# Optimization experiments

Measured on AMD Instinct MI355X. Metric: run time of the kernel, lower is better.

The kernel has to match this reference:

```python
import jax, jax.numpy as jnp
import numpy as np

N_H = 256
N_LAYERS = 3
D_IN = 2  # concat([t, x], axis=1)


def setup_inputs() -> dict:
    key = jax.random.key(0)
    ks = jax.random.split(key, 20)
    N = 131072
    H, L = N_H, N_LAYERS

    def xavier(k, shape):
        fan_in, fan_out = shape[-2], shape[-1]
        limit = np.sqrt(6.0 / (fan_in + fan_out)).astype(np.float32)
        return jax.random.uniform(k, shape, jnp.float32, -limit, limit)

    inp = {
        "t": jax.random.uniform(ks[0], (N, 1), jnp.float32),
        "x": jax.random.normal(ks[1], (N, 1), jnp.float32),
        # initial dense layer: [2, H]
        "W0": xavier(ks[2], (D_IN, H)),
        "b0": jnp.zeros((1, H), jnp.float32),
        # stacked per-layer LSTM-like weights: U* [L, 2, H], W* [L, H, H], b* [L, 1, H]
        "Uz": xavier(ks[3], (L, D_IN, H)),
        "Ug": xavier(ks[4], (L, D_IN, H)),
        "Ur": xavier(ks[5], (L, D_IN, H)),
        "Uh": xavier(ks[6], (L, D_IN, H)),
        "Wz": xavier(ks[7], (L, H, H)),
        "Wg": xavier(ks[8], (L, H, H)),
        "Wr": xavier(ks[9], (L, H, H)),
        "Wh": xavier(ks[10], (L, H, H)),
        "bz": jnp.zeros((L, 1, H), jnp.float32),
        "bg": jnp.zeros((L, 1, H), jnp.float32),
        "br": jnp.zeros((L, 1, H), jnp.float32),
        "bh": jnp.zeros((L, 1, H), jnp.float32),
        # final dense layer: [H, 1]
        "Wf": xavier(ks[11], (H, 1)),
        "bf": jnp.zeros((1, 1), jnp.float32),
    }
    return inp


def _dgm_forward(t, x, W0, b0, Uz, Ug, Ur, Uh, Wz, Wg, Wr, Wh, bz, bg, br, bh, Wf, bf):
    X = jnp.concatenate([t, x], axis=1)            # [N, 2]
    S1 = jnp.tanh(X @ W0 + b0)                     # [N, H] -- initial state, held fixed

    def layer_step(S, params):
        uz, ug, ur, uh, wz, wg, wr, wh, pz, pg, pr, ph = params
        Z = jnp.tanh(X @ uz + S @ wz + pz)
        G = jnp.tanh(X @ ug + S1 @ wg + pg)
        R = jnp.tanh(X @ ur + S @ wr + pr)
        Hg = jnp.tanh(X @ uh + (S * R) @ wh + ph)
        Snew = (1.0 - G) * Hg + Z * S
        return Snew, None

    S, _ = jax.lax.scan(layer_step, S1, (Uz, Ug, Ur, Uh, Wz, Wg, Wr, Wh, bz, bg, br, bh))
    return S @ Wf + bf                             # [N, 1]


def reference(t, x, W0, b0, Uz, Ug, Ur, Uh, Wz, Wg, Wr, Wh, bz, bg, br, bh, Wf, bf):
    return _dgm_forward(t, x, W0, b0, Uz, Ug, Ur, Uh, Wz, Wg, Wr, Wh, bz, bg, br, bh, Wf, bf)
```

## Files before the change

### kernel.cpp

```cpp
#include <hip/hip_runtime.h>


typedef __attribute__((ext_vector_type(8))) short bf16x8;
typedef __attribute__((ext_vector_type(4))) float f32x4;

#if __has_builtin(__builtin_amdgcn_exp2f)
#define EXP2F(x) __builtin_amdgcn_exp2f(x)
#else
#define EXP2F(x) __expf((x) * 0.6931471805599453f)
#endif

__device__ __forceinline__ short f2bf(float f) {
    unsigned u = __float_as_uint(f);
    unsigned r = (u + 0x7FFFu + ((u >> 16) & 1u)) >> 16;
    return (short)r;
}
__device__ __forceinline__ float bf2f(short h) {
    return __uint_as_float(((unsigned)(unsigned short)h) << 16);
}
__device__ __forceinline__ unsigned cvtpk(float lo, float hi) {
    unsigned r;
    asm("v_cvt_pk_bf16_f32 %0, %1, %2" : "=v"(r) : "v"(lo), "v"(hi));
    return r;
}
__device__ __forceinline__ float rcp_1pe2x(float x) {
    float e = EXP2F(x * 2.8853900817779268f);
    return __builtin_amdgcn_rcpf(e + 1.0f);
}
__device__ __forceinline__ float fast_tanh(float x) {
    return fmaf(-2.0f, rcp_1pe2x(x), 1.0f);
}
__device__ __forceinline__ int sw_off(int r, int k) {
    return r * 256 + ((((k >> 3) ^ r) & 31) << 3) + (k & 7);
}
__device__ __forceinline__ unsigned pk2(float a, float b) { return cvtpk(a, b); }
__device__ __forceinline__ float upk(unsigned p, int hi) {
    return __uint_as_float(hi ? (p & 0xFFFF0000u) : (p << 16));
}

__global__ void pack_w(const float* __restrict__ Wz, const float* __restrict__ Wg,
                       const float* __restrict__ Wr, const float* __restrict__ Wh,
                       short* __restrict__ out) {
    __shared__ __align__(16) short lds[256 * 40];
    int mat = blockIdx.x >> 3;
    int kb  = blockIdx.x & 7;
    int l = mat >> 2, g = mat & 3;
    const float* W = (g == 0) ? Wz : (g == 1) ? Wg : (g == 2) ? Wr : Wh;
    const float* Wsl = W + l * 65536 + kb * 32 * 256;
    const int t = threadIdx.x;

#pragma unroll
    for (int j = 0; j < 8; j++) {
        int f  = j * 256 + t;
        int kp = f >> 6;
        int n0 = (f & 63) * 4;
        float4 v = ((const float4*)Wsl)[f];
        lds[(n0 + 0) * 40 + kp] = f2bf(v.x);
        lds[(n0 + 1) * 40 + kp] = f2bf(v.y);
        lds[(n0 + 2) * 40 + kp] = f2bf(v.z);
        lds[(n0 + 3) * 40 + kp] = f2bf(v.w);
    }
    __syncthreads();

    short* outm = out + mat * 65536;
#pragma unroll
    for (int j = 0; j < 4; j++) {
        int vp = j * 256 + t;
        int c  = vp >> 6;
        int ln = vp & 63;
        int n   = c * 16 + (ln & 15);
        int kp0 = (ln >> 4) * 8;
        bf16x8 val = *(const bf16x8*)(lds + n * 40 + kp0);
        *(bf16x8*)(outm + (((c * 8 + kb) * 64 + ln) << 3)) = val;
    }
}

__device__ __forceinline__ void gate_gemm(const short* __restrict__ In,
                                          const short* __restrict__ Wm,
                                          const float* __restrict__ U,
                                          const float* __restrict__ bias,
                                          const float2* __restrict__ txS,
                                          int q, int c15, int w,
                                          f32x4 acc[2][2]) {
    float2 tx[8];
#pragma unroll
    for (int rb = 0; rb < 2; rb++)
#pragma unroll
        for (int ii = 0; ii < 4; ii++) tx[rb * 4 + ii] = txS[rb * 16 + q * 4 + ii];
#pragma unroll
    for (int cb = 0; cb < 2; cb++) {
        int col = (w * 2 + cb) * 16 + c15;
        float u0 = U[col], u1 = U[256 + col], bb = bias[col];
#pragma unroll
        for (int rb = 0; rb < 2; rb++)
#pragma unroll
            for (int ii = 0; ii < 4; ii++)
                acc[rb][cb][ii] = bb + tx[rb * 4 + ii].x * u0 + tx[rb * 4 + ii].y * u1;
    }
    __builtin_amdgcn_s_setprio(1);
#pragma unroll
    for (int kb = 0; kb < 8; kb++) {
        bf16x8 a[2];
#pragma unroll
        for (int rb = 0; rb < 2; rb++) {
            int r = rb * 16 + c15;
            a[rb] = *(const bf16x8*)(In + r * 256 + ((((kb * 4 + q) ^ r) & 31) << 3));
        }
#pragma unroll
        for (int cb = 0; cb < 2; cb++) {
            bf16x8 b = *(const bf16x8*)(Wm + ((((w * 2 + cb) * 8 + kb) * 64 + (q * 16 + c15)) << 3));
#pragma unroll
            for (int rb = 0; rb < 2; rb++)
                acc[rb][cb] = __builtin_amdgcn_mfma_f32_16x16x32_bf16(a[rb], b, acc[rb][cb], 0, 0, 0);
        }
    }
    __builtin_amdgcn_s_setprio(0);
}

__global__ __launch_bounds__(512, 4)
void dgm_main(const float* __restrict__ T, const float* __restrict__ X,
              const float* __restrict__ W0, const float* __restrict__ b0,
              const float* __restrict__ Uz, const float* __restrict__ Ug,
              const float* __restrict__ Ur, const float* __restrict__ Uh,
              const float* __restrict__ bz, const float* __restrict__ bg,
              const float* __restrict__ br, const float* __restrict__ bh,
              const float* __restrict__ Wf, const float* __restrict__ bfp,
              const short* __restrict__ Wp, float* __restrict__ out) {
    __shared__ __align__(16) short Sb[8192];
    __shared__ __align__(16) short S1b[8192];
    __shared__ float2 txS[32];

    const int tid = threadIdx.x;
    const int w   = tid >> 6;
    const int ln  = tid & 63;
    const int q   = ln >> 4;
    const int c15 = ln & 15;
    const int m0  = blockIdx.x * 32;

    if (tid < 32) txS[tid] = make_float2(T[m0 + tid], X[m0 + tid]);
    __syncthreads();

    {
        int col  = tid & 255;
        int half = tid >> 8;
        float w00 = W0[col], w01 = W0[256 + col], bb = b0[col];
#pragma unroll 4
        for (int rr = 0; rr < 16; rr++) {
            int r = half * 16 + rr;
            float2 tx = txS[r];
            short v = f2bf(fast_tanh(tx.x * w00 + tx.y * w01 + bb));
            int off = sw_off(r, col);
            S1b[off] = v;
            Sb[off]  = v;
        }
    }
    __syncthreads();

    unsigned sreg[2][2][2];
#pragma unroll
    for (int rb = 0; rb < 2; rb++)
#pragma unroll
        for (int cb = 0; cb < 2; cb++) {
            int col = (w * 2 + cb) * 16 + c15;
#pragma unroll
            for (int p = 0; p < 2; p++) {
                unsigned lo = (unsigned short)Sb[sw_off(rb * 16 + q * 4 + 2 * p,     col)];
                unsigned hi = (unsigned short)Sb[sw_off(rb * 16 + q * 4 + 2 * p + 1, col)];
                sreg[rb][cb][p] = lo | (hi << 16);
            }
        }

    for (int l = 0; l < 3; l++) {
        const short* Wzp = Wp + (l * 4 + 0) * 65536;
        const short* Wgp = Wp + (l * 4 + 1) * 65536;
        const short* Wrp = Wp + (l * 4 + 2) * 65536;
        const short* Whp = Wp + (l * 4 + 3) * 65536;

        f32x4 acc[2][2];
        unsigned zsp[2][2][2], srp[2][2][2], gmp[2][2][2];

        gate_gemm(Sb, Wzp, Uz + l * 512, bz + l * 256, txS, q, c15, w, acc);
#pragma unroll
        for (int rb = 0; rb < 2; rb++)
#pragma unroll
            for (int cb = 0; cb < 2; cb++)
#pragma unroll
                for (int p = 0; p < 2; p++)
                    zsp[rb][cb][p] = pk2(
                        fast_tanh(acc[rb][cb][2 * p])     * upk(sreg[rb][cb][p], 0),
                        fast_tanh(acc[rb][cb][2 * p + 1]) * upk(sreg[rb][cb][p], 1));

        gate_gemm(Sb, Wrp, Ur + l * 512, br + l * 256, txS, q, c15, w, acc);
#pragma unroll
        for (int rb = 0; rb < 2; rb++)
#pragma unroll
            for (int cb = 0; cb < 2; cb++)
#pragma unroll
                for (int p = 0; p < 2; p++)
                    srp[rb][cb][p] = pk2(
                        upk(sreg[rb][cb][p], 0) * fast_tanh(acc[rb][cb][2 * p]),
                        upk(sreg[rb][cb][p], 1) * fast_tanh(acc[rb][cb][2 * p + 1]));

        gate_gemm(S1b, Wgp, Ug + l * 512, bg + l * 256, txS, q, c15, w, acc);
#pragma unroll
        for (int rb = 0; rb < 2; rb++)
#pragma unroll
            for (int cb = 0; cb < 2; cb++)
#pragma unroll
                for (int p = 0; p < 2; p++)
                    gmp[rb][cb][p] = pk2(2.0f * rcp_1pe2x(acc[rb][cb][2 * p]),
                                         2.0f * rcp_1pe2x(acc[rb][cb][2 * p + 1]));

        __syncthreads();
#pragma unroll
        for (int rb = 0; rb < 2; rb++)
#pragma unroll
            for (int cb = 0; cb < 2; cb++) {
                int col = (w * 2 + cb) * 16 + c15;
#pragma unroll
                for (int p = 0; p < 2; p++) {
                    Sb[sw_off(rb * 16 + q * 4 + 2 * p,     col)] = (short)(srp[rb][cb][p] & 0xFFFFu);
                    Sb[sw_off(rb * 16 + q * 4 + 2 * p + 1, col)] = (short)(srp[rb][cb][p] >> 16);
                }
            }
        __syncthreads();

        gate_gemm(Sb, Whp, Uh + l * 512, bh + l * 256, txS, q, c15, w, acc);

#pragma unroll
        for (int rb = 0; rb < 2; rb++)
#pragma unroll
            for (int cb = 0; cb < 2; cb++)
#pragma unroll
                for (int p = 0; p < 2; p++) {
                    float sn0 = fmaf(upk(gmp[rb][cb][p], 0),
                                     fast_tanh(acc[rb][cb][2 * p]),
                                     upk(zsp[rb][cb][p], 0));
                    float sn1 = fmaf(upk(gmp[rb][cb][p], 1),
                                     fast_tanh(acc[rb][cb][2 * p + 1]),
                                     upk(zsp[rb][cb][p], 1));
                    srp[rb][cb][p] = pk2(sn0, sn1);
                }

        __syncthreads();
#pragma unroll
        for (int rb = 0; rb < 2; rb++)
#pragma unroll
            for (int cb = 0; cb < 2; cb++) {
                int col = (w * 2 + cb) * 16 + c15;
#pragma unroll
                for (int p = 0; p < 2; p++) {
                    Sb[sw_off(rb * 16 + q * 4 + 2 * p,     col)] = (short)(srp[rb][cb][p] & 0xFFFFu);
                    Sb[sw_off(rb * 16 + q * 4 + 2 * p + 1, col)] = (short)(srp[rb][cb][p] >> 16);
                    sreg[rb][cb][p] = srp[rb][cb][p];
                }
            }
        __syncthreads();
    }

    {
        int row = tid >> 4;
        int seg = tid & 15;
        float sum = 0.0f;
#pragma unroll
        for (int j = 0; j < 2; j++) {
            int ch = seg * 2 + j;
            bf16x8 sv = *(const bf16x8*)(Sb + row * 256 + (((ch ^ row) & 31) << 3));
            float4 wa = *(const float4*)(Wf + ch * 8);
            float4 wb = *(const float4*)(Wf + ch * 8 + 4);
            sum += bf2f(sv[0]) * wa.x + bf2f(sv[1]) * wa.y + bf2f(sv[2]) * wa.z + bf2f(sv[3]) * wa.w
                 + bf2f(sv[4]) * wb.x + bf2f(sv[5]) * wb.y + bf2f(sv[6]) * wb.z + bf2f(sv[7]) * wb.w;
        }
        sum += __shfl_down(sum, 8, 16);
        sum += __shfl_down(sum, 4, 16);
        sum += __shfl_down(sum, 2, 16);
        sum += __shfl_down(sum, 1, 16);
        if (seg == 0) out[m0 + row] = sum + bfp[0];
    }
}

extern "C" void kernel_launch(void* const* d_in, const int* in_sizes, int n_in,
                              void* d_out, int out_size, void* d_ws, size_t ws_size,
                              hipStream_t stream) {
    const float* T  = (const float*)d_in[0];
    const float* X  = (const float*)d_in[1];
    const float* W0 = (const float*)d_in[2];
    const float* b0 = (const float*)d_in[3];
    const float* Uz = (const float*)d_in[4];
    const float* Ug = (const float*)d_in[5];
    const float* Ur = (const float*)d_in[6];
    const float* Uh = (const float*)d_in[7];
    const float* Wz = (const float*)d_in[8];
    const float* Wg = (const float*)d_in[9];
    const float* Wr = (const float*)d_in[10];
    const float* Wh = (const float*)d_in[11];
    const float* bz = (const float*)d_in[12];
    const float* bg = (const float*)d_in[13];
    const float* br = (const float*)d_in[14];
    const float* bh = (const float*)d_in[15];
    const float* Wf = (const float*)d_in[16];
    const float* bfp= (const float*)d_in[17];
    float* out = (float*)d_out;
    short* Wp = (short*)d_ws;
    const int N = in_sizes[0];

    pack_w<<<96, 256, 0, stream>>>(Wz, Wg, Wr, Wh, Wp);
    dgm_main<<<N / 32, 512, 0, stream>>>(T, X, W0, b0, Uz, Ug, Ur, Uh,
                                         bz, bg, br, bh, Wf, bfp, Wp, out);
}
```

Before: 417.3 us.

## Split block work across 16 waves with one column tile per wave

Doubles the block size from 512 to 1024 threads so each of 16 waves owns a single 16-column tile instead of two, halving per-thread accumulators and packed state. The initial tanh layer and the final dot-product reduction are re-partitioned to match the larger block. This aims to raise latency hiding and cut register pressure. The cost is more waves contending at each block barrier, each wave re-reading the same A fragments from LDS (so more LDS traffic per MFMA), and the launch bound claiming 8 waves per SIMD, which may not fit.

```diff
diff --git a/kernel.cpp b/kernel.cpp
--- a/kernel.cpp
+++ b/kernel.cpp
@@ -81,22 +81,16 @@
                                           const float* __restrict__ bias,
                                           const float2* __restrict__ txS,
                                           int q, int c15, int w,
-                                          f32x4 acc[2][2]) {
-    float2 tx[8];
+                                          f32x4 acc[2]) {
+    int col = w * 16 + c15;
+    float u0 = U[col], u1 = U[256 + col], bb = bias[col];
 #pragma unroll
     for (int rb = 0; rb < 2; rb++)
 #pragma unroll
-        for (int ii = 0; ii < 4; ii++) tx[rb * 4 + ii] = txS[rb * 16 + q * 4 + ii];
-#pragma unroll
-    for (int cb = 0; cb < 2; cb++) {
-        int col = (w * 2 + cb) * 16 + c15;
-        float u0 = U[col], u1 = U[256 + col], bb = bias[col];
-#pragma unroll
-        for (int rb = 0; rb < 2; rb++)
-#pragma unroll
-            for (int ii = 0; ii < 4; ii++)
-                acc[rb][cb][ii] = bb + tx[rb * 4 + ii].x * u0 + tx[rb * 4 + ii].y * u1;
-    }
+        for (int ii = 0; ii < 4; ii++) {
+            float2 t2 = txS[rb * 16 + q * 4 + ii];
+            acc[rb][ii] = bb + t2.x * u0 + t2.y * u1;
+        }
     __builtin_amdgcn_s_setprio(1);
 #pragma unroll
     for (int kb = 0; kb < 8; kb++) {
@@ -106,18 +100,15 @@
             int r = rb * 16 + c15;
             a[rb] = *(const bf16x8*)(In + r * 256 + ((((kb * 4 + q) ^ r) & 31) << 3));
         }
-#pragma unroll
-        for (int cb = 0; cb < 2; cb++) {
-            bf16x8 b = *(const bf16x8*)(Wm + ((((w * 2 + cb) * 8 + kb) * 64 + (q * 16 + c15)) << 3));
-#pragma unroll
-            for (int rb = 0; rb < 2; rb++)
-                acc[rb][cb] = __builtin_amdgcn_mfma_f32_16x16x32_bf16(a[rb], b, acc[rb][cb], 0, 0, 0);
-        }
+        bf16x8 b = *(const bf16x8*)(Wm + (((w * 8 + kb) * 64 + (q * 16 + c15)) << 3));
+#pragma unroll
+        for (int rb = 0; rb < 2; rb++)
+            acc[rb] = __builtin_amdgcn_mfma_f32_16x16x32_bf16(a[rb], b, acc[rb], 0, 0, 0);
     }
     __builtin_amdgcn_s_setprio(0);
 }
 
-__global__ __launch_bounds__(512, 4)
+__global__ __launch_bounds__(1024, 8)
 void dgm_main(const float* __restrict__ T, const float* __restrict__ X,
               const float* __restrict__ W0, const float* __restrict__ b0,
               const float* __restrict__ Uz, const float* __restrict__ Ug,
@@ -141,12 +132,12 @@
     __syncthreads();
 
     {
-        int col  = tid & 255;
-        int half = tid >> 8;
+        int col = tid & 255;
+        int qt  = tid >> 8;
         float w00 = W0[col], w01 = W0[256 + col], bb = b0[col];
-#pragma unroll 4
-        for (int rr = 0; rr < 16; rr++) {
-            int r = half * 16 + rr;
+#pragma unroll
+        for (int rr = 0; rr < 8; rr++) {
+            int r = qt * 8 + rr;
             float2 tx = txS[r];
             short v = f2bf(fast_tanh(tx.x * w00 + tx.y * w01 + bb));
             int off = sw_off(r, col);
@@ -156,18 +147,16 @@
     }
     __syncthreads();
 
-    unsigned sreg[2][2][2];
+    const int colw = w * 16 + c15;
+
+    unsigned sreg[2][2];
 #pragma unroll
     for (int rb = 0; rb < 2; rb++)
 #pragma unroll
-        for (int cb = 0; cb < 2; cb++) {
-            int col = (w * 2 + cb) * 16 + c15;
-#pragma unroll
-            for (int p = 0; p < 2; p++) {
-                unsigned lo = (unsigned short)Sb[sw_off(rb * 16 + q * 4 + 2 * p,     col)];
-                unsigned hi = (unsigned short)Sb[sw_off(rb * 16 + q * 4 + 2 * p + 1, col)];
-                sreg[rb][cb][p] = lo | (hi << 16);
-            }
+        for (int p = 0; p < 2; p++) {
+            unsigned lo = (unsigned short)Sb[sw_off(rb * 16 + q * 4 + 2 * p,     colw)];
+            unsigned hi = (unsigned short)Sb[sw_off(rb * 16 + q * 4 + 2 * p + 1, colw)];
+            sreg[rb][p] = lo | (hi << 16);
         }
 
     for (int l = 0; l < 3; l++) {
@@ -176,52 +165,42 @@
         const short* Wrp = Wp + (l * 4 + 2) * 65536;
         const short* Whp = Wp + (l * 4 + 3) * 65536;
 
-        f32x4 acc[2][2];
-        unsigned zsp[2][2][2], srp[2][2][2], gmp[2][2][2];
+        f32x4 acc[2];
+        unsigned zsp[2][2], srp[2][2], gmp[2][2];
 
         gate_gemm(Sb, Wzp, Uz + l * 512, bz + l * 256, txS, q, c15, w, acc);
 #pragma unroll
         for (int rb = 0; rb < 2; rb++)
 #pragma unroll
-            for (int cb = 0; cb < 2; cb++)
-#pragma unroll
-                for (int p = 0; p < 2; p++)
-                    zsp[rb][cb][p] = pk2(
-                        fast_tanh(acc[rb][cb][2 * p])     * upk(sreg[rb][cb][p], 0),
-                        fast_tanh(acc[rb][cb][2 * p + 1]) * upk(sreg[rb][cb][p], 1));
+            for (int p = 0; p < 2; p++)
+                zsp[rb][p] = pk2(
+                    fast_tanh(acc[rb][2 * p])     * upk(sreg[rb][p], 0),
+                    fast_tanh(acc[rb][2 * p + 1]) * upk(sreg[rb][p], 1));
 
         gate_gemm(Sb, Wrp, Ur + l * 512, br + l * 256, txS, q, c15, w, acc);
 #pragma unroll
         for (int rb = 0; rb < 2; rb++)
 #pragma unroll
-            for (int cb = 0; cb < 2; cb++)
-#pragma unroll
-                for (int p = 0; p < 2; p++)
-                    srp[rb][cb][p] = pk2(
-                        upk(sreg[rb][cb][p], 0) * fast_tanh(acc[rb][cb][2 * p]),
-                        upk(sreg[rb][cb][p], 1) * fast_tanh(acc[rb][cb][2 * p + 1]));
+            for (int p = 0; p < 2; p++)
+                srp[rb][p] = pk2(
+                    upk(sreg[rb][p], 0) * fast_tanh(acc[rb][2 * p]),
+                    upk(sreg[rb][p], 1) * fast_tanh(acc[rb][2 * p + 1]));
 
         gate_gemm(S1b, Wgp, Ug + l * 512, bg + l * 256, txS, q, c15, w, acc);
 #pragma unroll
         for (int rb = 0; rb < 2; rb++)
 #pragma unroll
-            for (int cb = 0; cb < 2; cb++)
-#pragma unroll
-                for (int p = 0; p < 2; p++)
-                    gmp[rb][cb][p] = pk2(2.0f * rcp_1pe2x(acc[rb][cb][2 * p]),
-                                         2.0f * rcp_1pe2x(acc[rb][cb][2 * p + 1]));
-
-        __syncthreads();
-#pragma unroll
-        for (int rb = 0; rb < 2; rb++)
-#pragma unroll
-            for (int cb = 0; cb < 2; cb++) {
-                int col = (w * 2 + cb) * 16 + c15;
-#pragma unroll
-                for (int p = 0; p < 2; p++) {
-                    Sb[sw_off(rb * 16 + q * 4 + 2 * p,     col)] = (short)(srp[rb][cb][p] & 0xFFFFu);
-                    Sb[sw_off(rb * 16 + q * 4 + 2 * p + 1, col)] = (short)(srp[rb][cb][p] >> 16);
-                }
+            for (int p = 0; p < 2; p++)
+                gmp[rb][p] = pk2(2.0f * rcp_1pe2x(acc[rb][2 * p]),
+                                 2.0f * rcp_1pe2x(acc[rb][2 * p + 1]));
+
+        __syncthreads();
+#pragma unroll
+        for (int rb = 0; rb < 2; rb++)
+#pragma unroll
+            for (int p = 0; p < 2; p++) {
+                Sb[sw_off(rb * 16 + q * 4 + 2 * p,     colw)] = (short)(srp[rb][p] & 0xFFFFu);
+                Sb[sw_off(rb * 16 + q * 4 + 2 * p + 1, colw)] = (short)(srp[rb][p] >> 16);
             }
         __syncthreads();
 
@@ -230,51 +209,41 @@
 #pragma unroll
         for (int rb = 0; rb < 2; rb++)
 #pragma unroll
-            for (int cb = 0; cb < 2; cb++)
-#pragma unroll
-                for (int p = 0; p < 2; p++) {
-                    float sn0 = fmaf(upk(gmp[rb][cb][p], 0),
-                                     fast_tanh(acc[rb][cb][2 * p]),
-                                     upk(zsp[rb][cb][p], 0));
-                    float sn1 = fmaf(upk(gmp[rb][cb][p], 1),
-                                     fast_tanh(acc[rb][cb][2 * p + 1]),
-                                     upk(zsp[rb][cb][p], 1));
-                    srp[rb][cb][p] = pk2(sn0, sn1);
-                }
-
-        __syncthreads();
-#pragma unroll
-        for (int rb = 0; rb < 2; rb++)
-#pragma unroll
-            for (int cb = 0; cb < 2; cb++) {
-                int col = (w * 2 + cb) * 16 + c15;
-#pragma unroll
-                for (int p = 0; p < 2; p++) {
-                    Sb[sw_off(rb * 16 + q * 4 + 2 * p,     col)] = (short)(srp[rb][cb][p] & 0xFFFFu);
-                    Sb[sw_off(rb * 16 + q * 4 + 2 * p + 1, col)] = (short)(srp[rb][cb][p] >> 16);
-                    sreg[rb][cb][p] = srp[rb][cb][p];
-                }
+            for (int p = 0; p < 2; p++) {
+                float sn0 = fmaf(upk(gmp[rb][p], 0),
+                                 fast_tanh(acc[rb][2 * p]),
+                                 upk(zsp[rb][p], 0));
+                float sn1 = fmaf(upk(gmp[rb][p], 1),
+                                 fast_tanh(acc[rb][2 * p + 1]),
+                                 upk(zsp[rb][p], 1));
+                srp[rb][p] = pk2(sn0, sn1);
             }
+
+        __syncthreads();
+#pragma unroll
+        for (int rb = 0; rb < 2; rb++)
+#pragma unroll
+            for (int p = 0; p < 2; p++) {
+                Sb[sw_off(rb * 16 + q * 4 + 2 * p,     colw)] = (short)(srp[rb][p] & 0xFFFFu);
+                Sb[sw_off(rb * 16 + q * 4 + 2 * p + 1, colw)] = (short)(srp[rb][p] >> 16);
+                sreg[rb][p] = srp[rb][p];
+            }
         __syncthreads();
     }
 
     {
-        int row = tid >> 4;
-        int seg = tid & 15;
-        float sum = 0.0f;
-#pragma unroll
-        for (int j = 0; j < 2; j++) {
-            int ch = seg * 2 + j;
-            bf16x8 sv = *(const bf16x8*)(Sb + row * 256 + (((ch ^ row) & 31) << 3));
-            float4 wa = *(const float4*)(Wf + ch * 8);
-            float4 wb = *(const float4*)(Wf + ch * 8 + 4);
-            sum += bf2f(sv[0]) * wa.x + bf2f(sv[1]) * wa.y + bf2f(sv[2]) * wa.z + bf2f(sv[3]) * wa.w
-                 + bf2f(sv[4]) * wb.x + bf2f(sv[5]) * wb.y + bf2f(sv[6]) * wb.z + bf2f(sv[7]) * wb.w;
-        }
-        sum += __shfl_down(sum, 8, 16);
-        sum += __shfl_down(sum, 4, 16);
-        sum += __shfl_down(sum, 2, 16);
-        sum += __shfl_down(sum, 1, 16);
+        int row = tid >> 5;
+        int seg = tid & 31;
+        bf16x8 sv = *(const bf16x8*)(Sb + row * 256 + (((seg ^ row) & 31) << 3));
+        float4 wa = *(const float4*)(Wf + seg * 8);
+        float4 wb = *(const float4*)(Wf + seg * 8 + 4);
+        float sum = bf2f(sv[0]) * wa.x + bf2f(sv[1]) * wa.y + bf2f(sv[2]) * wa.z + bf2f(sv[3]) * wa.w
+                  + bf2f(sv[4]) * wb.x + bf2f(sv[5]) * wb.y + bf2f(sv[6]) * wb.z + bf2f(sv[7]) * wb.w;
+        sum += __shfl_down(sum, 16, 32);
+        sum += __shfl_down(sum, 8, 32);
+        sum += __shfl_down(sum, 4, 32);
+        sum += __shfl_down(sum, 2, 32);
+        sum += __shfl_down(sum, 1, 32);
         if (seg == 0) out[m0 + row] = sum + bfp[0];
     }
 }
@@ -305,6 +274,6 @@
     const int N = in_sizes[0];
 
     pack_w<<<96, 256, 0, stream>>>(Wz, Wg, Wr, Wh, Wp);
-    dgm_main<<<N / 32, 512, 0, stream>>>(T, X, W0, b0, Uz, Ug, Ur, Uh,
-                                         bz, bg, br, bh, Wf, bfp, Wp, out);
-}
+    dgm_main<<<N / 32, 1024, 0, stream>>>(T, X, W0, b0, Uz, Ug, Ur, Uh,
+                                          bz, bg, br, bh, Wf, bfp, Wp, out);
+}
```

Result: slower. 595.1 us (+42.6%).
